# Kernel optimization log

Measured on AMD Instinct MI355X. Metric: run time of the kernel, lower is better.

Reference implementation:

```python
import jax, jax.numpy as jnp
import numpy as np

N_NODES = 50000
N_EDGES = 800000
D_IN = 128
D_HID = 128
D_OUT = 128


def _sage_conv(x, row, col, Wl, Wr, b):
    # PyG SAGEConv (mean aggregation, root weight, bias):
    # out = mean_{j in N(i)} x_j @ Wl^T + x_i @ Wr^T + b
    n = x.shape[0]
    msg = x[col]                                            # [E, D] gather from source nodes
    agg = jax.ops.segment_sum(msg, row, num_segments=n)     # [N, D]
    deg = jax.ops.segment_sum(jnp.ones((row.shape[0],), x.dtype), row, num_segments=n)
    agg = agg / jnp.maximum(deg, 1.0)[:, None]
    return agg @ Wl.T + x @ Wr.T + b


def setup_inputs() -> dict:
    key = jax.random.key(0)
    ks = jax.random.split(key, 12)
    x = jax.random.normal(ks[0], (N_NODES, D_IN), dtype=jnp.float32)
    edge_row = jax.random.randint(ks[1], (N_EDGES,), 0, N_NODES)
    edge_col = jax.random.randint(ks[2], (N_EDGES,), 0, N_NODES)
    dims = [(D_HID, D_IN), (D_HID, D_HID), (D_OUT, D_HID)]
    inp = {"x": x, "edge_row": edge_row, "edge_col": edge_col}
    for i, (do, di) in enumerate(dims):
        s = 1.0 / np.sqrt(di)
        inp[f"Wl{i}"] = jax.random.uniform(ks[3 + 3 * i], (do, di), jnp.float32, -s, s)
        inp[f"Wr{i}"] = jax.random.uniform(ks[4 + 3 * i], (do, di), jnp.float32, -s, s)
        inp[f"b{i}"] = jax.random.uniform(ks[5 + 3 * i], (do,), jnp.float32, -s, s)
    return inp


def reference(x, edge_row, edge_col, Wl0, Wr0, b0, Wl1, Wr1, b1, Wl2, Wr2, b2):
    # Single branch (num_layers=[3]), use_res=True, dropout=0 (eval mode).
    params = [(Wl0, Wr0, b0), (Wl1, Wr1, b1), (Wl2, Wr2, b2)]
    x1 = _sage_conv(x, edge_row, edge_col, *params[0])
    for Wl, Wr, b in params[1:]:
        x2 = x1
        x1 = jax.nn.relu(x1)
        x1 = _sage_conv(x1, edge_row, edge_col, Wl, Wr, b) + x2
    # x_final = sum(branches) / number; one branch -> divide by 1
    return x1 / 1.0
```

## Files before the change

kernel.cpp:

```cpp
#include <hip/hip_runtime.h>

#define NN 50000
#define NE 800000
#define D  128

typedef _Float16 f16;
typedef _Float16 f16x4 __attribute__((ext_vector_type(4)));
typedef _Float16 f16x8 __attribute__((ext_vector_type(8)));
typedef float f32x4 __attribute__((ext_vector_type(4)));
typedef float f32x2 __attribute__((ext_vector_type(2)));
typedef unsigned short u16;
typedef unsigned int u32;
typedef unsigned char u8;

#define NB   64
#define ECH  12500
#define NHW  12500

__global__ __launch_bounds__(1024) void prep_hist(
    const float* __restrict__ x, f16* __restrict__ xf, u8* __restrict__ xf8,
    const float* w0, const float* w1, const float* w2,
    const float* w3, const float* w4, const float* w5,
    f16* d0, f16* d1, f16* d2, f16* d3, f16* d4, f16* d5,
    const int* __restrict__ erow, u32* __restrict__ histw,
    u16* __restrict__ lrank, int* __restrict__ cursor) {
    __shared__ u32 lh[NHW];
    int b = blockIdx.x;
    const int tid = threadIdx.x;
    if (b < NB) {
        for (int w = tid; w < NHW; w += 1024) lh[w] = 0;
        if (b == 0 && tid == 0) *cursor = 0;
        __syncthreads();
        const int base = b * ECH;
        for (int k = tid; k < ECH; k += 1024) {
            int e = base + k;
            int r = erow[e];
            int sh = (r & 3) * 8;
            u32 old = atomicAdd(&lh[r >> 2], 1u << sh);
            lrank[e] = (u16)((old >> sh) & 0xffu);
        }
        __syncthreads();
        u32* hb = histw + b * NHW;
        for (int w = tid; w < NHW; w += 1024) hb[w] = lh[w];
    } else if (b < NB + 1563) {
        int i = (b - NB) * 1024 + tid;
        if (i < NN * D / 4) {
            float4 v = ((const float4*)x)[i];
            f16x4 o = {(f16)v.x, (f16)v.y, (f16)v.z, (f16)v.w};
            ((f16x4*)xf)[i] = o;
            u32 lo = __builtin_amdgcn_cvt_pk_fp8_f32(v.x, v.y, 0, false);
            u32 pk = __builtin_amdgcn_cvt_pk_fp8_f32(v.z, v.w, lo, true);
            ((u32*)xf8)[i] = pk;
        }
    } else {
        int wb = b - (NB + 1563);
        int mat = wb >> 2;
        const float* s; f16* d;
        switch (mat) {
            case 0: s = w0; d = d0; break; case 1: s = w1; d = d1; break;
            case 2: s = w2; d = d2; break; case 3: s = w3; d = d3; break;
            case 4: s = w4; d = d4; break; default: s = w5; d = d5; break;
        }
        int i = (wb & 3) * 1024 + tid;
        float4 v = ((const float4*)s)[i];
        f16x4 o = {(f16)v.x, (f16)v.y, (f16)v.z, (f16)v.w};
        ((f16x4*)d)[i] = o;
    }
}

__global__ __launch_bounds__(256) void scan_cols_off(
    const u32* __restrict__ histw, u16* __restrict__ start16,
    int* __restrict__ deg, int* __restrict__ cursor,
    int* __restrict__ offsets) {
    __shared__ int wsum[4];
    __shared__ int bbase;
    const int tid = threadIdx.x;
    const int w = tid >> 6, lane = tid & 63;
    const int n = blockIdx.x * 256 + tid;

    int s = 0;
    if (n < NN) {
        int sh = (n & 3) * 8;
        for (int b = 0; b < NB; ++b) {
            u32 wv = histw[b * NHW + (n >> 2)];
            start16[b * NN + n] = (u16)s;
            s += (int)((wv >> sh) & 0xffu);
        }
        deg[n] = s;
    }
    int v = s;
    int x = v;
#pragma unroll
    for (int m = 1; m < 64; m <<= 1) {
        int t = __shfl_up(x, m, 64);
        if (lane >= m) x += t;
    }
    if (lane == 63) wsum[w] = x;
    __syncthreads();
    if (w == 0) {
        int t = (lane < 4) ? wsum[lane] : 0;
#pragma unroll
        for (int m = 1; m < 4; m <<= 1) {
            int u = __shfl_up(t, m, 64);
            if (lane >= m) t += u;
        }
        if (lane < 4) wsum[lane] = t;
        if (lane == 3) bbase = atomicAdd(cursor, t);
    }
    __syncthreads();
    int excl = x - v + (w ? wsum[w - 1] : 0);
    if (n < NN) offsets[n] = bbase + excl;
}

__global__ __launch_bounds__(256) void fill_csr(
    const int* __restrict__ row, const int* __restrict__ col,
    const u16* __restrict__ lrank, const u16* __restrict__ start16,
    const int* __restrict__ offsets, u16* __restrict__ csr_col) {
    int i = blockIdx.x * 256 + threadIdx.x;
    int r = row[i];
    int b = i / ECH;
    int p = offsets[r] + (int)start16[b * NN + r] + (int)lrank[i];
    csr_col[p] = (u16)col[i];
}

__global__ __launch_bounds__(256) void aggregate_f8(
    const u8* __restrict__ h8, const int* __restrict__ offsets,
    const int* __restrict__ degv, const u16* __restrict__ csr,
    f16* __restrict__ agg) {
    int node = blockIdx.x * 4 + (threadIdx.x >> 6);
    int lane = threadIdx.x & 63;
    int sub = lane >> 4, fl = lane & 15;
    int s0 = offsets[node];
    int deg = degv[node];

    int cl = 0;
    if (lane < deg) cl = (int)csr[s0 + lane];

    float acc[8];
#pragma unroll
    for (int u = 0; u < 8; ++u) acc[u] = 0.f;

    const u8* hp = h8 + fl * 8;

#define UNPACK_ADD(vv)                                                 \
    do {                                                               \
        f32x2 p;                                                       \
        p = __builtin_amdgcn_cvt_pk_f32_fp8((vv).x, false);            \
        acc[0] += p.x; acc[1] += p.y;                                  \
        p = __builtin_amdgcn_cvt_pk_f32_fp8((vv).x, true);             \
        acc[2] += p.x; acc[3] += p.y;                                  \
        p = __builtin_amdgcn_cvt_pk_f32_fp8((vv).y, false);            \
        acc[4] += p.x; acc[5] += p.y;                                  \
        p = __builtin_amdgcn_cvt_pk_f32_fp8((vv).y, true);             \
        acc[6] += p.x; acc[7] += p.y;                                  \
    } while (0)

    int ng = (deg <= 64) ? deg : 64;
    int e = sub;
    for (int it = ng >> 4; it > 0; --it, e += 16) {
        int c0 = __shfl(cl, e, 64);
        int c1 = __shfl(cl, e + 4, 64);
        int c2 = __shfl(cl, e + 8, 64);
        int c3 = __shfl(cl, e + 12, 64);
        uint2 g0 = *(const uint2*)(hp + (size_t)c0 * D);
        uint2 g1 = *(const uint2*)(hp + (size_t)c1 * D);
        uint2 g2 = *(const uint2*)(hp + (size_t)c2 * D);
        uint2 g3 = *(const uint2*)(hp + (size_t)c3 * D);
        UNPACK_ADD(g0);
        UNPACK_ADD(g1);
        UNPACK_ADD(g2);
        UNPACK_ADD(g3);
    }
    if (ng & 8) {
        int c0 = __shfl(cl, e, 64);
        int c1 = __shfl(cl, e + 4, 64);
        uint2 g0 = *(const uint2*)(hp + (size_t)c0 * D);
        uint2 g1 = *(const uint2*)(hp + (size_t)c1 * D);
        UNPACK_ADD(g0);
        UNPACK_ADD(g1);
        e += 8;
    }
    if (ng & 4) {
        int c = __shfl(cl, e, 64);
        uint2 g = *(const uint2*)(hp + (size_t)c * D);
        UNPACK_ADD(g);
        e += 4;
    }
    {
        int r = ng & 3;
        if (r) {
            int ec = (e < ng) ? e : (ng - 1);
            int c = __shfl(cl, ec, 64);
            if (sub < r) {
                uint2 g = *(const uint2*)(hp + (size_t)c * D);
                UNPACK_ADD(g);
            }
        }
    }
    if (deg > 64) {
        for (int j = s0 + 64 + sub; j < s0 + deg; j += 4) {
            int c = (int)csr[j];
            uint2 g = *(const uint2*)(hp + (size_t)c * D);
            UNPACK_ADD(g);
        }
    }
#undef UNPACK_ADD

#pragma unroll
    for (int u = 0; u < 8; ++u) {
        acc[u] += __shfl_xor(acc[u], 16, 64);
        acc[u] += __shfl_xor(acc[u], 32, 64);
    }
    if (sub == 0) {
        float inv = 1.f / fmaxf((float)deg, 1.f);
        f16x8 o;
#pragma unroll
        for (int u = 0; u < 8; ++u) o[u] = (f16)(acc[u] * inv);
        *((f16x8*)(agg + (size_t)node * D) + fl) = o;
    }
}

#define WPAD 72

template<int RELU_X, int ADD_RES, int OUT_F32>
__global__ __launch_bounds__(256, 4) void sage_gemm_mfma(
    const f16* __restrict__ aggb, const f16* __restrict__ xb,
    const f16* __restrict__ Wl, const f16* __restrict__ Wr,
    const float* __restrict__ bias, float* __restrict__ outf,
    f16* __restrict__ outh, u8* __restrict__ out8) {
    __shared__ f16 sW[2][128][WPAD];

    const int tid  = threadIdx.x;
    const int wave = tid >> 6;
    const int lane = tid & 63;
    const int lm = lane & 15;
    const int q  = lane >> 4;
    const int mt = blockIdx.x * 64 + wave * 16;

    int row = mt + lm;
    int rclamp = (row < NN) ? row : NN - 1;

    f16x8 Aa[4], Ax[4];
    const f16* arow = aggb + (size_t)rclamp * D + q * 8;
    const f16* xrow = xb  + (size_t)rclamp * D + q * 8;
#pragma unroll
    for (int ks = 0; ks < 4; ++ks) {
        Aa[ks] = *(const f16x8*)(arow + ks * 32);
        f16x8 v = *(const f16x8*)(xrow + ks * 32);
        if (RELU_X) {
#pragma unroll
            for (int u = 0; u < 8; ++u) v[u] = (v[u] < (f16)0) ? (f16)0 : v[u];
        }
        Ax[ks] = v;
    }

    f32x4 acc[8];
#pragma unroll
    for (int nt = 0; nt < 8; ++nt) acc[nt] = (f32x4){0.f, 0.f, 0.f, 0.f};

    for (int p = 0; p < 2; ++p) {
        __syncthreads();
#pragma unroll
        for (int it = 0; it < 8; ++it) {
            int idx = tid + it * 256;
            int mat = idx >> 10;
            int n   = (idx >> 3) & 127;
            int c   = idx & 7;
            const f16* W = mat ? Wr : Wl;
            f16x8 v = *(const f16x8*)(W + n * D + p * 64 + c * 8);
            *(f16x8*)&sW[mat][n][c * 8] = v;
        }
        __syncthreads();

#pragma unroll
        for (int nt = 0; nt < 8; ++nt) {
#pragma unroll
            for (int k2 = 0; k2 < 2; ++k2) {
                f16x8 bl = *(const f16x8*)&sW[0][nt * 16 + lm][k2 * 32 + q * 8];
                acc[nt] = __builtin_amdgcn_mfma_f32_16x16x32_f16(Aa[p * 2 + k2], bl, acc[nt], 0, 0, 0);
                f16x8 br = *(const f16x8*)&sW[1][nt * 16 + lm][k2 * 32 + q * 8];
                acc[nt] = __builtin_amdgcn_mfma_f32_16x16x32_f16(Ax[p * 2 + k2], br, acc[nt], 0, 0, 0);
            }
        }
    }

#pragma unroll
    for (int nt = 0; nt < 8; ++nt) {
        int n = nt * 16 + lm;
        float bval = bias[n];
#pragma unroll
        for (int r = 0; r < 4; ++r) {
            int m = mt + q * 4 + r;
            if (m < NN) {
                size_t idx = (size_t)m * D + n;
                float v = acc[nt][r] + bval;
                if (ADD_RES) v += (float)xb[idx];
                if (OUT_F32) {
                    outf[idx] = v;
                } else {
                    outh[idx] = (f16)v;
                    u32 t = __builtin_amdgcn_cvt_pk_fp8_f32(fmaxf(v, 0.f), 0.f, 0, false);
                    out8[idx] = (u8)(t & 0xffu);
                }
            }
        }
    }
}


extern "C" void kernel_launch(void* const* d_in, const int* in_sizes, int n_in,
                              void* d_out, int out_size, void* d_ws, size_t ws_size,
                              hipStream_t stream) {
    const float* x    = (const float*)d_in[0];
    const int*   erow = (const int*)d_in[1];
    const int*   ecol = (const int*)d_in[2];
    const float* Wl0 = (const float*)d_in[3];
    const float* Wr0 = (const float*)d_in[4];
    const float* b0  = (const float*)d_in[5];
    const float* Wl1 = (const float*)d_in[6];
    const float* Wr1 = (const float*)d_in[7];
    const float* b1  = (const float*)d_in[8];
    const float* Wl2 = (const float*)d_in[9];
    const float* Wr2 = (const float*)d_in[10];
    const float* b2  = (const float*)d_in[11];

    char* ws = (char*)d_ws;
    size_t off = 0;
    auto carve = [&](size_t bytes) -> void* {
        void* p = ws + off;
        off = (off + bytes + 255) & ~(size_t)255;
        return p;
    };
    int*   deg     = (int*)carve((size_t)(NN + 1) * 4);
    int*   offsets = (int*)carve((size_t)NN * 4);
    u32*   histw   = (u32*)carve((size_t)NB * NHW * 4);
    u16*   start16 = (u16*)carve((size_t)NB * NN * 2);
    u16*   lrank   = (u16*)carve((size_t)NE * 2);
    u16*   csr_col = (u16*)carve((size_t)NE * 2);
    f16*   xf      = (f16*)carve((size_t)NN * D * 2);
    f16*   x1      = (f16*)carve((size_t)NN * D * 2);
    f16*   aggb    = (f16*)carve((size_t)NN * D * 2);
    u8*    xf8     = (u8*)carve((size_t)NN * D);
    u8*    x1f8    = (u8*)carve((size_t)NN * D);
    f16*   wl0 = (f16*)carve(D * D * 2); f16* wr0 = (f16*)carve(D * D * 2);
    f16*   wl1 = (f16*)carve(D * D * 2); f16* wr1 = (f16*)carve(D * D * 2);
    f16*   wl2 = (f16*)carve(D * D * 2); f16* wr2 = (f16*)carve(D * D * 2);
    (void)ws_size; (void)in_sizes; (void)n_in; (void)out_size;

    float* outp = (float*)d_out;

    prep_hist<<<NB + 1563 + 24, 1024, 0, stream>>>(
        x, xf, xf8, Wl0, Wr0, Wl1, Wr1, Wl2, Wr2,
        wl0, wr0, wl1, wr1, wl2, wr2, erow, histw, lrank, deg + NN);
    scan_cols_off<<<(NN + 255) / 256, 256, 0, stream>>>(histw, start16, deg,
                                                        deg + NN, offsets);
    fill_csr<<<NE / 256, 256, 0, stream>>>(erow, ecol, lrank, start16, offsets, csr_col);

    const int agrid = NN / 4;
    const int ggrid = (NN + 63) / 64;

    aggregate_f8<<<agrid, 256, 0, stream>>>(xf8, offsets, deg, csr_col, aggb);
    sage_gemm_mfma<0, 0, 0><<<ggrid, 256, 0, stream>>>(aggb, xf, wl0, wr0, b0,
                                                       nullptr, x1, x1f8);
    aggregate_f8<<<agrid, 256, 0, stream>>>(x1f8, offsets, deg, csr_col, aggb);
    sage_gemm_mfma<1, 1, 0><<<ggrid, 256, 0, stream>>>(aggb, x1, wl1, wr1, b1,
                                                       nullptr, x1, x1f8);
    aggregate_f8<<<agrid, 256, 0, stream>>>(x1f8, offsets, deg, csr_col, aggb);
    sage_gemm_mfma<1, 1, 1><<<ggrid, 256, 0, stream>>>(aggb, x1, wl2, wr2, b2,
                                                       outp, nullptr, nullptr);
}
```

Measured before the change: 243.9 us.

## Fuse neighbor aggregation and SAGE GEMM into one kernel per layer

Merges the per-layer fp8 gather/mean aggregation kernel and the MFMA GEMM kernel into a single kernel. Each 256-thread block aggregates 16 nodes into shared memory and then multiplies them against Wl/Wr staged in LDS. This removes the fp16 aggregation buffer round trip through global memory and three kernel launches. In exchange, each of the many small blocks reloads the full weight matrices into LDS, and each wave now aggregates four nodes one after another. The fp8 feature buffers now ping-pong between layers so the in-place update stays safe.

```diff
diff --git a/kernel.cpp b/kernel.cpp
--- a/kernel.cpp
+++ b/kernel.cpp
@@ -123,24 +123,36 @@
     csr_col[p] = (u16)col[i];
 }
 
-__global__ __launch_bounds__(256) void aggregate_f8(
+#define WPAD 72
+#define AP   136
+
+template<int RELU_X, int ADD_RES, int OUT_F32>
+__global__ __launch_bounds__(256) void sage_layer(
     const u8* __restrict__ h8, const int* __restrict__ offsets,
     const int* __restrict__ degv, const u16* __restrict__ csr,
-    f16* __restrict__ agg) {
-    int node = blockIdx.x * 4 + (threadIdx.x >> 6);
-    int lane = threadIdx.x & 63;
-    int sub = lane >> 4, fl = lane & 15;
-    int s0 = offsets[node];
-    int deg = degv[node];
-
-    int cl = 0;
-    if (lane < deg) cl = (int)csr[s0 + lane];
-
-    float acc[8];
-#pragma unroll
-    for (int u = 0; u < 8; ++u) acc[u] = 0.f;
-
-    const u8* hp = h8 + fl * 8;
+    const f16* __restrict__ xb,
+    const f16* __restrict__ Wl, const f16* __restrict__ Wr,
+    const float* __restrict__ bias, float* __restrict__ outf,
+    f16* __restrict__ outh, u8* __restrict__ out8) {
+    __shared__ f16 sW[2][128][WPAD];
+    __shared__ f16 aggT[16][AP];
+
+    const int tid  = threadIdx.x;
+    const int wave = tid >> 6;
+    const int lane = tid & 63;
+    const int sub = lane >> 4, fl = lane & 15;
+    const int mb = blockIdx.x * 16;
+
+#pragma unroll
+    for (int it = 0; it < 8; ++it) {
+        int idx = tid + it * 256;
+        int mat = idx >> 10;
+        int n   = (idx >> 3) & 127;
+        int c   = idx & 7;
+        const f16* W = mat ? Wr : Wl;
+        f16x8 v = *(const f16x8*)(W + n * D + c * 8);
+        *(f16x8*)&sW[mat][n][c * 8] = v;
+    }
 
 #define UNPACK_ADD(vv)                                                 \
     do {                                                               \
@@ -155,153 +167,178 @@
         acc[6] += p.x; acc[7] += p.y;                                  \
     } while (0)
 
-    int ng = (deg <= 64) ? deg : 64;
-    int e = sub;
-    for (int it = ng >> 4; it > 0; --it, e += 16) {
-        int c0 = __shfl(cl, e, 64);
-        int c1 = __shfl(cl, e + 4, 64);
-        int c2 = __shfl(cl, e + 8, 64);
-        int c3 = __shfl(cl, e + 12, 64);
-        uint2 g0 = *(const uint2*)(hp + (size_t)c0 * D);
-        uint2 g1 = *(const uint2*)(hp + (size_t)c1 * D);
-        uint2 g2 = *(const uint2*)(hp + (size_t)c2 * D);
-        uint2 g3 = *(const uint2*)(hp + (size_t)c3 * D);
-        UNPACK_ADD(g0);
-        UNPACK_ADD(g1);
-        UNPACK_ADD(g2);
-        UNPACK_ADD(g3);
-    }
-    if (ng & 8) {
-        int c0 = __shfl(cl, e, 64);
-        int c1 = __shfl(cl, e + 4, 64);
-        uint2 g0 = *(const uint2*)(hp + (size_t)c0 * D);
-        uint2 g1 = *(const uint2*)(hp + (size_t)c1 * D);
-        UNPACK_ADD(g0);
-        UNPACK_ADD(g1);
-        e += 8;
-    }
-    if (ng & 4) {
-        int c = __shfl(cl, e, 64);
-        uint2 g = *(const uint2*)(hp + (size_t)c * D);
-        UNPACK_ADD(g);
-        e += 4;
-    }
-    {
-        int r = ng & 3;
-        if (r) {
-            int ec = (e < ng) ? e : (ng - 1);
-            int c = __shfl(cl, ec, 64);
-            if (sub < r) {
+    const u8* hp = h8 + fl * 8;
+#pragma unroll 1
+    for (int i = 0; i < 4; ++i) {
+        int node = mb + wave * 4 + i;
+        int s0  = offsets[node];
+        int deg = degv[node];
+        int cl = 0;
+        if (lane < deg) cl = (int)csr[s0 + lane];
+
+        float acc[8];
+#pragma unroll
+        for (int u = 0; u < 8; ++u) acc[u] = 0.f;
+
+        int ng = (deg <= 64) ? deg : 64;
+        int e = sub;
+        for (int it = ng >> 4; it > 0; --it, e += 16) {
+            int c0 = __shfl(cl, e, 64);
+            int c1 = __shfl(cl, e + 4, 64);
+            int c2 = __shfl(cl, e + 8, 64);
+            int c3 = __shfl(cl, e + 12, 64);
+            uint2 g0 = *(const uint2*)(hp + (size_t)c0 * D);
+            uint2 g1 = *(const uint2*)(hp + (size_t)c1 * D);
+            uint2 g2 = *(const uint2*)(hp + (size_t)c2 * D);
+            uint2 g3 = *(const uint2*)(hp + (size_t)c3 * D);
+            UNPACK_ADD(g0);
+            UNPACK_ADD(g1);
+            UNPACK_ADD(g2);
+            UNPACK_ADD(g3);
+        }
+        if (ng & 8) {
+            int c0 = __shfl(cl, e, 64);
+            int c1 = __shfl(cl, e + 4, 64);
+            uint2 g0 = *(const uint2*)(hp + (size_t)c0 * D);
+            uint2 g1 = *(const uint2*)(hp + (size_t)c1 * D);
+            UNPACK_ADD(g0);
+            UNPACK_ADD(g1);
+            e += 8;
+        }
+        if (ng & 4) {
+            int c = __shfl(cl, e, 64);
+            uint2 g = *(const uint2*)(hp + (size_t)c * D);
+            UNPACK_ADD(g);
+            e += 4;
+        }
+        {
+            int r = ng & 3;
+            if (r) {
+                int ec = (e < ng) ? e : (ng - 1);
+                int c = __shfl(cl, ec, 64);
+                if (sub < r) {
+                    uint2 g = *(const uint2*)(hp + (size_t)c * D);
+                    UNPACK_ADD(g);
+                }
+            }
+        }
+        if (deg > 64) {
+            for (int jj = s0 + 64 + sub; jj < s0 + deg; jj += 4) {
+                int c = (int)csr[jj];
                 uint2 g = *(const uint2*)(hp + (size_t)c * D);
                 UNPACK_ADD(g);
             }
         }
-    }
-    if (deg > 64) {
-        for (int j = s0 + 64 + sub; j < s0 + deg; j += 4) {
-            int c = (int)csr[j];
-            uint2 g = *(const uint2*)(hp + (size_t)c * D);
-            UNPACK_ADD(g);
+
+#pragma unroll
+        for (int u = 0; u < 8; ++u) {
+            acc[u] += __shfl_xor(acc[u], 16, 64);
+            acc[u] += __shfl_xor(acc[u], 32, 64);
+        }
+        if (sub == 0) {
+            float inv = 1.f / fmaxf((float)deg, 1.f);
+            f16x8 o;
+#pragma unroll
+            for (int u = 0; u < 8; ++u) o[u] = (f16)(acc[u] * inv);
+            *(f16x8*)&aggT[wave * 4 + i][fl * 8] = o;
         }
     }
 #undef UNPACK_ADD
 
-#pragma unroll
-    for (int u = 0; u < 8; ++u) {
-        acc[u] += __shfl_xor(acc[u], 16, 64);
-        acc[u] += __shfl_xor(acc[u], 32, 64);
-    }
-    if (sub == 0) {
-        float inv = 1.f / fmaxf((float)deg, 1.f);
-        f16x8 o;
-#pragma unroll
-        for (int u = 0; u < 8; ++u) o[u] = (f16)(acc[u] * inv);
-        *((f16x8*)(agg + (size_t)node * D) + fl) = o;
-    }
-}
-
-#define WPAD 72
-
-template<int RELU_X, int ADD_RES, int OUT_F32>
-__global__ __launch_bounds__(256, 4) void sage_gemm_mfma(
-    const f16* __restrict__ aggb, const f16* __restrict__ xb,
-    const f16* __restrict__ Wl, const f16* __restrict__ Wr,
-    const float* __restrict__ bias, float* __restrict__ outf,
-    f16* __restrict__ outh, u8* __restrict__ out8) {
-    __shared__ f16 sW[2][128][WPAD];
-
-    const int tid  = threadIdx.x;
-    const int wave = tid >> 6;
-    const int lane = tid & 63;
-    const int lm = lane & 15;
-    const int q  = lane >> 4;
-    const int mt = blockIdx.x * 64 + wave * 16;
-
-    int row = mt + lm;
-    int rclamp = (row < NN) ? row : NN - 1;
-
-    f16x8 Aa[4], Ax[4];
-    const f16* arow = aggb + (size_t)rclamp * D + q * 8;
-    const f16* xrow = xb  + (size_t)rclamp * D + q * 8;
-#pragma unroll
-    for (int ks = 0; ks < 4; ++ks) {
-        Aa[ks] = *(const f16x8*)(arow + ks * 32);
-        f16x8 v = *(const f16x8*)(xrow + ks * 32);
+    __syncthreads();
+
+    const int lm = fl, q = sub;
+    const int nt0 = wave * 2;
+    const f16* xrow = xb + (size_t)(mb + lm) * D + q * 8;
+    f32x4 acc0 = (f32x4){0.f, 0.f, 0.f, 0.f};
+    f32x4 acc1 = (f32x4){0.f, 0.f, 0.f, 0.f};
+
+    {
+        f16x8 Aa0 = *(const f16x8*)&aggT[lm][q * 8];
+        f16x8 Aa1 = *(const f16x8*)&aggT[lm][32 + q * 8];
+        f16x8 Ax0 = *(const f16x8*)(xrow);
+        f16x8 Ax1 = *(const f16x8*)(xrow + 32);
         if (RELU_X) {
 #pragma unroll
-            for (int u = 0; u < 8; ++u) v[u] = (v[u] < (f16)0) ? (f16)0 : v[u];
-        }
-        Ax[ks] = v;
-    }
-
-    f32x4 acc[8];
-#pragma unroll
-    for (int nt = 0; nt < 8; ++nt) acc[nt] = (f32x4){0.f, 0.f, 0.f, 0.f};
-
-    for (int p = 0; p < 2; ++p) {
-        __syncthreads();
-#pragma unroll
-        for (int it = 0; it < 8; ++it) {
-            int idx = tid + it * 256;
-            int mat = idx >> 10;
-            int n   = (idx >> 3) & 127;
-            int c   = idx & 7;
-            const f16* W = mat ? Wr : Wl;
-            f16x8 v = *(const f16x8*)(W + n * D + p * 64 + c * 8);
-            *(f16x8*)&sW[mat][n][c * 8] = v;
-        }
-        __syncthreads();
-
-#pragma unroll
-        for (int nt = 0; nt < 8; ++nt) {
-#pragma unroll
-            for (int k2 = 0; k2 < 2; ++k2) {
-                f16x8 bl = *(const f16x8*)&sW[0][nt * 16 + lm][k2 * 32 + q * 8];
-                acc[nt] = __builtin_amdgcn_mfma_f32_16x16x32_f16(Aa[p * 2 + k2], bl, acc[nt], 0, 0, 0);
-                f16x8 br = *(const f16x8*)&sW[1][nt * 16 + lm][k2 * 32 + q * 8];
-                acc[nt] = __builtin_amdgcn_mfma_f32_16x16x32_f16(Ax[p * 2 + k2], br, acc[nt], 0, 0, 0);
+            for (int u = 0; u < 8; ++u) {
+                Ax0[u] = (Ax0[u] < (f16)0) ? (f16)0 : Ax0[u];
+                Ax1[u] = (Ax1[u] < (f16)0) ? (f16)0 : Ax1[u];
             }
         }
-    }
-
-#pragma unroll
-    for (int nt = 0; nt < 8; ++nt) {
-        int n = nt * 16 + lm;
+#pragma unroll
+        for (int j = 0; j < 2; ++j) {
+            int n = (nt0 + j) * 16 + lm;
+            f16x8 bl0 = *(const f16x8*)&sW[0][n][q * 8];
+            f16x8 br0 = *(const f16x8*)&sW[1][n][q * 8];
+            f16x8 bl1 = *(const f16x8*)&sW[0][n][32 + q * 8];
+            f16x8 br1 = *(const f16x8*)&sW[1][n][32 + q * 8];
+            f32x4 a = j ? acc1 : acc0;
+            a = __builtin_amdgcn_mfma_f32_16x16x32_f16(Aa0, bl0, a, 0, 0, 0);
+            a = __builtin_amdgcn_mfma_f32_16x16x32_f16(Ax0, br0, a, 0, 0, 0);
+            a = __builtin_amdgcn_mfma_f32_16x16x32_f16(Aa1, bl1, a, 0, 0, 0);
+            a = __builtin_amdgcn_mfma_f32_16x16x32_f16(Ax1, br1, a, 0, 0, 0);
+            if (j) acc1 = a; else acc0 = a;
+        }
+    }
+
+    __syncthreads();
+#pragma unroll
+    for (int it = 0; it < 8; ++it) {
+        int idx = tid + it * 256;
+        int mat = idx >> 10;
+        int n   = (idx >> 3) & 127;
+        int c   = idx & 7;
+        const f16* W = mat ? Wr : Wl;
+        f16x8 v = *(const f16x8*)(W + n * D + 64 + c * 8);
+        *(f16x8*)&sW[mat][n][c * 8] = v;
+    }
+    __syncthreads();
+
+    {
+        f16x8 Aa2 = *(const f16x8*)&aggT[lm][64 + q * 8];
+        f16x8 Aa3 = *(const f16x8*)&aggT[lm][96 + q * 8];
+        f16x8 Ax2 = *(const f16x8*)(xrow + 64);
+        f16x8 Ax3 = *(const f16x8*)(xrow + 96);
+        if (RELU_X) {
+#pragma unroll
+            for (int u = 0; u < 8; ++u) {
+                Ax2[u] = (Ax2[u] < (f16)0) ? (f16)0 : Ax2[u];
+                Ax3[u] = (Ax3[u] < (f16)0) ? (f16)0 : Ax3[u];
+            }
+        }
+#pragma unroll
+        for (int j = 0; j < 2; ++j) {
+            int n = (nt0 + j) * 16 + lm;
+            f16x8 bl0 = *(const f16x8*)&sW[0][n][q * 8];
+            f16x8 br0 = *(const f16x8*)&sW[1][n][q * 8];
+            f16x8 bl1 = *(const f16x8*)&sW[0][n][32 + q * 8];
+            f16x8 br1 = *(const f16x8*)&sW[1][n][32 + q * 8];
+            f32x4 a = j ? acc1 : acc0;
+            a = __builtin_amdgcn_mfma_f32_16x16x32_f16(Aa2, bl0, a, 0, 0, 0);
+            a = __builtin_amdgcn_mfma_f32_16x16x32_f16(Ax2, br0, a, 0, 0, 0);
+            a = __builtin_amdgcn_mfma_f32_16x16x32_f16(Aa3, bl1, a, 0, 0, 0);
+            a = __builtin_amdgcn_mfma_f32_16x16x32_f16(Ax3, br1, a, 0, 0, 0);
+            if (j) acc1 = a; else acc0 = a;
+        }
+    }
+
+#pragma unroll
+    for (int j = 0; j < 2; ++j) {
+        int n = (nt0 + j) * 16 + lm;
         float bval = bias[n];
+        f32x4 a = j ? acc1 : acc0;
 #pragma unroll
         for (int r = 0; r < 4; ++r) {
-            int m = mt + q * 4 + r;
-            if (m < NN) {
-                size_t idx = (size_t)m * D + n;
-                float v = acc[nt][r] + bval;
-                if (ADD_RES) v += (float)xb[idx];
-                if (OUT_F32) {
-                    outf[idx] = v;
-                } else {
-                    outh[idx] = (f16)v;
-                    u32 t = __builtin_amdgcn_cvt_pk_fp8_f32(fmaxf(v, 0.f), 0.f, 0, false);
-                    out8[idx] = (u8)(t & 0xffu);
-                }
+            int m = mb + q * 4 + r;
+            size_t idx = (size_t)m * D + n;
+            float v = a[r] + bval;
+            if (ADD_RES) v += (float)xb[idx];
+            if (OUT_F32) {
+                outf[idx] = v;
+            } else {
+                outh[idx] = (f16)v;
+                u32 t = __builtin_amdgcn_cvt_pk_fp8_f32(fmaxf(v, 0.f), 0.f, 0, false);
+                out8[idx] = (u8)(t & 0xffu);
             }
         }
     }
@@ -339,7 +376,6 @@
     u16*   csr_col = (u16*)carve((size_t)NE * 2);
     f16*   xf      = (f16*)carve((size_t)NN * D * 2);
     f16*   x1      = (f16*)carve((size_t)NN * D * 2);
-    f16*   aggb    = (f16*)carve((size_t)NN * D * 2);
     u8*    xf8     = (u8*)carve((size_t)NN * D);
     u8*    x1f8    = (u8*)carve((size_t)NN * D);
     f16*   wl0 = (f16*)carve(D * D * 2); f16* wr0 = (f16*)carve(D * D * 2);
@@ -356,16 +392,12 @@
                                                         deg + NN, offsets);
     fill_csr<<<NE / 256, 256, 0, stream>>>(erow, ecol, lrank, start16, offsets, csr_col);
 
-    const int agrid = NN / 4;
-    const int ggrid = (NN + 63) / 64;
-
-    aggregate_f8<<<agrid, 256, 0, stream>>>(xf8, offsets, deg, csr_col, aggb);
-    sage_gemm_mfma<0, 0, 0><<<ggrid, 256, 0, stream>>>(aggb, xf, wl0, wr0, b0,
-                                                       nullptr, x1, x1f8);
-    aggregate_f8<<<agrid, 256, 0, stream>>>(x1f8, offsets, deg, csr_col, aggb);
-    sage_gemm_mfma<1, 1, 0><<<ggrid, 256, 0, stream>>>(aggb, x1, wl1, wr1, b1,
-                                                       nullptr, x1, x1f8);
-    aggregate_f8<<<agrid, 256, 0, stream>>>(x1f8, offsets, deg, csr_col, aggb);
-    sage_gemm_mfma<1, 1, 1><<<ggrid, 256, 0, stream>>>(aggb, x1, wl2, wr2, b2,
-                                                       outp, nullptr, nullptr);
+    const int lgrid = NN / 16;
+
+    sage_layer<0, 0, 0><<<lgrid, 256, 0, stream>>>(
+        xf8, offsets, deg, csr_col, xf, wl0, wr0, b0, nullptr, x1, x1f8);
+    sage_layer<1, 1, 0><<<lgrid, 256, 0, stream>>>(
+        x1f8, offsets, deg, csr_col, x1, wl1, wr1, b1, nullptr, x1, xf8);
+    sage_layer<1, 1, 1><<<lgrid, 256, 0, stream>>>(
+        xf8, offsets, deg, csr_col, x1, wl2, wr2, b2, outp, nullptr, nullptr);
 }
```

New measurement: 290.5 us. +19.1%, slower.
